# Optimization experiments

Measured on AMD Instinct MI355X. Metric: run time of the kernel, lower is better.

## Reference

```python
import jax, jax.numpy as jnp
import numpy as np

N_EMBD = 1024
N_HEAD = 16
DIM_HEAD = N_EMBD // N_HEAD
SCALE = DIM_HEAD ** (-0.5)  # NOTE: module DIVIDES by this (multiplies by sqrt(d)) - kept faithful


def setup_inputs() -> dict:
    key = jax.random.key(0)
    ks = jax.random.split(key, 6)
    B, Tq, Tkv = 2, 2048, 2048
    x_q = jax.random.normal(ks[0], (B, Tq, N_EMBD), dtype=jnp.float32)
    x_kv = jax.random.normal(ks[1], (B, Tkv, N_EMBD), dtype=jnp.float32)
    position_bias = jax.random.normal(ks[2], (1, N_HEAD, Tq, Tkv), dtype=jnp.float32)
    s = 0.02
    W_q = jax.random.normal(ks[3], (N_EMBD, N_EMBD), dtype=jnp.float32) * s
    W_kv = jax.random.normal(ks[4], (N_EMBD, 2 * N_EMBD), dtype=jnp.float32) * s
    W_proj = jax.random.normal(ks[5], (N_EMBD, N_EMBD), dtype=jnp.float32) * s
    return {"x_q": x_q, "x_kv": x_kv, "position_bias": position_bias,
            "W_q": W_q, "W_kv": W_kv, "W_proj": W_proj}


def reference(x_q, x_kv, position_bias, W_q, W_kv, W_proj):
    B, Tq, C = x_q.shape
    Tkv = x_kv.shape[1]
    q = x_q @ W_q                       # [B,Tq,C]
    kv = x_kv @ W_kv                    # [B,Tkv,2C]
    k, v = kv[..., :C], kv[..., C:]
    # split heads -> [B,H,T,dh]
    q = q.reshape(B, Tq, N_HEAD, DIM_HEAD).transpose(0, 2, 1, 3)
    k = k.reshape(B, Tkv, N_HEAD, DIM_HEAD).transpose(0, 2, 1, 3)
    v = v.reshape(B, Tkv, N_HEAD, DIM_HEAD).transpose(0, 2, 1, 3)
    attn = jnp.einsum('bhqd,bhkd->bhqk', q, k)
    attn = attn + position_bias
    attn = attn / SCALE  # faithful to source: divides by d**-0.5
    attn = jax.nn.softmax(attn, axis=-1)
    y = jnp.einsum('bhqk,bhkd->bhqd', attn, v)
    y = y.transpose(0, 2, 1, 3).reshape(B, Tq, C)
    return y @ W_proj
```

## Files before the change

### kernel.cpp

```cpp
#include <hip/hip_runtime.h>
#include <hip/hip_bf16.h>

#define TQ   2048
#define TKV  2048
#define NB   2
#define NH   16
#define HD   64
#define CE   1024
#define MQ   (NB*TQ)

typedef __bf16 bf16_t;
typedef __bf16 bf16x4_t __attribute__((ext_vector_type(4)));
typedef __bf16 bf16x8_t __attribute__((ext_vector_type(8)));
typedef float  f32x4_t  __attribute__((ext_vector_type(4)));

#define MFMA16(a,b,c) __builtin_amdgcn_mfma_f32_16x16x32_bf16((a),(b),(c),0,0,0)

__device__ __forceinline__ void gload16(const void* g, void* l) {
    __builtin_amdgcn_global_load_lds(
        (__attribute__((address_space(1))) void*)(void*)g,
        (__attribute__((address_space(3))) void*)l, 16, 0, 0);
}

__global__ __launch_bounds__(256) void cvt_split(const float* __restrict__ x,
                                                 bf16_t* __restrict__ hi,
                                                 bf16_t* __restrict__ lo, int n4) {
    int i = blockIdx.x * blockDim.x + threadIdx.x;
    int stride = gridDim.x * blockDim.x;
    for (; i < n4; i += stride) {
        f32x4_t v = ((const f32x4_t*)x)[i];
        bf16x4_t h, l;
#pragma unroll
        for (int j = 0; j < 4; j++) {
            h[j] = (bf16_t)v[j];
            l[j] = (bf16_t)(v[j] - (float)h[j]);
        }
        ((bf16x4_t*)hi)[i] = h;
        ((bf16x4_t*)lo)[i] = l;
    }
}

__global__ __launch_bounds__(256) void wsplit_t(const float* __restrict__ W,
                                                bf16_t* __restrict__ Wh,
                                                bf16_t* __restrict__ Wl, int K, int N) {
    __shared__ float t[32][33];
    int tx = threadIdx.x, ty = threadIdx.y;
    int n0 = blockIdx.x * 32, k0 = blockIdx.y * 32;
#pragma unroll
    for (int j = 0; j < 4; j++)
        t[ty + 8*j][tx] = W[(size_t)(k0 + ty + 8*j) * N + n0 + tx];
    __syncthreads();
#pragma unroll
    for (int j = 0; j < 4; j++) {
        float v = t[tx][ty + 8*j];
        bf16_t h = (bf16_t)v;
        Wh[(size_t)(n0 + ty + 8*j) * K + k0 + tx] = h;
        Wl[(size_t)(n0 + ty + 8*j) * K + k0 + tx] = (bf16_t)(v - (float)h);
    }
}

__global__ __launch_bounds__(256) void vtrans(const bf16_t* __restrict__ KVm,
                                              bf16_t* __restrict__ VT) {
    __shared__ bf16_t t[32][33];
    int tx = threadIdx.x, ty = threadIdx.y;
    int t0 = blockIdx.x * 32, d0 = blockIdx.y * 32, bh = blockIdx.z;
    int b = bh >> 4, h = bh & 15;
#pragma unroll
    for (int j = 0; j < 4; j++)
        t[ty + 8*j][tx] = KVm[(size_t)(b*TKV + t0 + ty + 8*j) * 2048 + 1024 + h*HD + d0 + tx];
    __syncthreads();
#pragma unroll
    for (int j = 0; j < 4; j++)
        VT[((size_t)bh*HD + d0 + ty + 8*j) * TKV + t0 + tx] = t[tx][ty + 8*j];
}

template <int PASSES, typename CT>
__device__ __forceinline__ void gemm_body(const bf16_t* __restrict__ Ah,
                                          const bf16_t* __restrict__ Al,
                                          const bf16_t* __restrict__ Bh,
                                          const bf16_t* __restrict__ Bl,
                                          CT* __restrict__ C,
                                          bf16_t* __restrict__ Clo,
                                          int bi, int bj, int N, int K, int Nlo,
                                          bf16_t* As, bf16_t* Bs, int tid) {
    int lane = tid & 63, w = tid >> 6;
    int wr = (w >> 1) * 64, wc = (w & 1) * 64;
    int lr = lane & 15, lg = lane >> 4;
    int row0 = tid >> 2, seg0 = tid & 3;

    f32x4_t acc[4][4];
#pragma unroll
    for (int m = 0; m < 4; m++)
#pragma unroll
        for (int n = 0; n < 4; n++)
            acc[m][n] = f32x4_t{0.f, 0.f, 0.f, 0.f};

    for (int p = 0; p < PASSES; ++p) {
        const bf16_t* Ap;
        const bf16_t* Bp;
        if (p == 0)      { Ap = Ah; Bp = Bh; }
        else if (p == 1) { if (PASSES == 3) { Ap = Ah; Bp = Bl; } else { Ap = Al; Bp = Bh; } }
        else             { Ap = Al; Bp = Bh; }
        for (int k0 = 0; k0 < K; k0 += 32) {
#pragma unroll
            for (int i = 0; i < 2; i++) {
                int row = row0 + i * 64;
                int sseg = seg0 ^ (row & 3);
                gload16(Ap + (size_t)(bi*128 + row) * K + k0 + sseg*8, (void*)(As + row*32 + seg0*8));
                gload16(Bp + (size_t)(bj*128 + row) * K + k0 + sseg*8, (void*)(Bs + row*32 + seg0*8));
            }
            __syncthreads();
            bf16x8_t af[4], bfr[4];
#pragma unroll
            for (int m = 0; m < 4; m++) {
                int ra = wr + m*16 + lr;
                af[m]  = *(const bf16x8_t*)(As + ra*32 + ((lg ^ (ra & 3)) * 8));
                int rb = wc + m*16 + lr;
                bfr[m] = *(const bf16x8_t*)(Bs + rb*32 + ((lg ^ (rb & 3)) * 8));
            }
#pragma unroll
            for (int m = 0; m < 4; m++)
#pragma unroll
                for (int n = 0; n < 4; n++)
                    acc[m][n] = MFMA16(af[m], bfr[n], acc[m][n]);
            __syncthreads();
        }
    }
#pragma unroll
    for (int m = 0; m < 4; m++) {
        int r = bi*128 + wr + m*16 + lg*4;
#pragma unroll
        for (int n = 0; n < 4; n++) {
            int c = bj*128 + wc + n*16 + lr;
#pragma unroll
            for (int i = 0; i < 4; i++) {
                float v = acc[m][n][i];
                if constexpr (__is_same(CT, float)) {
                    C[(size_t)(r + i) * N + c] = v;
                } else {
                    bf16_t h = (bf16_t)v;
                    C[(size_t)(r + i) * N + c] = h;
                    if (Clo && c < Nlo)
                        Clo[(size_t)(r + i) * Nlo + c] = (bf16_t)(v - (float)h);
                }
            }
        }
    }
}

__global__ __launch_bounds__(256) void gemm_qkv(const bf16_t* xqh, const bf16_t* xql,
                                                const bf16_t* wqh, const bf16_t* wql,
                                                bf16_t* q_hi, bf16_t* q_lo,
                                                const bf16_t* xkh, const bf16_t* xkl,
                                                const bf16_t* wkh, const bf16_t* wkl,
                                                bf16_t* kv_hi, bf16_t* k_lo) {
    __shared__ bf16_t As[128 * 32];
    __shared__ bf16_t Bs[128 * 32];
    int id = blockIdx.x, tid = threadIdx.x;
    if (id < 256) {
        gemm_body<3, bf16_t>(xqh, xql, wqh, wql, q_hi, q_lo,
                             id >> 3, id & 7, CE, CE, CE, As, Bs, tid);
    } else {
        id -= 256;
        gemm_body<3, bf16_t>(xkh, xkl, wkh, wkl, kv_hi, k_lo,
                             id >> 4, id & 15, 2048, CE, CE, As, Bs, tid);
    }
}

__global__ __launch_bounds__(256) void gemm_proj(const bf16_t* yh, const bf16_t* yl,
                                                 const bf16_t* wph,
                                                 float* out) {
    __shared__ bf16_t As[128 * 32];
    __shared__ bf16_t Bs[128 * 32];
    int id = blockIdx.x, tid = threadIdx.x;
    gemm_body<2, float>(yh, yl, wph, nullptr, out, nullptr,
                        id >> 3, id & 7, CE, CE, 0, As, Bs, tid);
}

__global__ __launch_bounds__(256, 2) void attn_fwd3(const bf16_t* __restrict__ Qh,
                                                    const bf16_t* __restrict__ Ql,
                                                    const bf16_t* __restrict__ KVh,
                                                    const bf16_t* __restrict__ Kl,
                                                    const bf16_t* __restrict__ VT,
                                                    const float*  __restrict__ Bias,
                                                    bf16_t* __restrict__ Yh,
                                                    bf16_t* __restrict__ Yl) {
    __shared__ bf16_t Kh_s[64 * 64];
    __shared__ bf16_t Kl_s[64 * 64];
    __shared__ bf16_t V_s [64 * 64];
    __shared__ bf16_t pb[4][32 * 72];

    int id = blockIdx.x;
    int swz = (id & 7) * 64 + (id >> 3);
    int qt = swz & 15, bh = swz >> 4;
    int b = bh >> 4, h = bh & 15;
    int tid = threadIdx.x, lane = tid & 63, w = tid >> 6;
    int lr = lane & 15, lg = lane >> 4;
    int q0 = qt * 128 + w * 32;

    bf16x8_t qhf[2][2], qlf[2][2];
#pragma unroll
    for (int qs = 0; qs < 2; qs++) {
        const bf16_t* qp = Qh + (size_t)(b*TQ + q0 + qs*16 + lr) * CE + h*HD + lg*8;
        const bf16_t* qp2 = Ql + (size_t)(b*TQ + q0 + qs*16 + lr) * CE + h*HD + lg*8;
        qhf[qs][0] = *(const bf16x8_t*)qp;
        qhf[qs][1] = *(const bf16x8_t*)(qp + 32);
        qlf[qs][0] = *(const bf16x8_t*)qp2;
        qlf[qs][1] = *(const bf16x8_t*)(qp2 + 32);
    }

    float m_r[2][4], l_r[2][4];
    f32x4_t oa[2][4];
#pragma unroll
    for (int qs = 0; qs < 2; qs++)
#pragma unroll
        for (int i = 0; i < 4; i++) {
            m_r[qs][i] = -1e30f; l_r[qs][i] = 0.f;
            oa[qs][i] = f32x4_t{0.f, 0.f, 0.f, 0.f};
        }

    bf16_t* myp = pb[w];
    const float*  bbase = Bias + ((size_t)h*TQ + q0 + lg*4) * TKV + lr;
    const bf16_t* khg = KVh + (size_t)(b*TKV) * 2048 + h*HD;
    const bf16_t* klg = Kl  + (size_t)(b*TKV) * 1024 + h*HD;
    const bf16_t* vtg = VT  + (size_t)bh * HD * TKV;

    for (int kv0 = 0; kv0 < TKV; kv0 += 64) {
#pragma unroll
        for (int s = 0; s < 2; s++) {
            int idx = s * 256 + tid;
            int row = idx >> 3;
            int sw  = (idx & 7) ^ (row & 7);
            gload16(khg + (size_t)(kv0 + row) * 2048 + sw*8, (void*)(Kh_s + idx*8));
            gload16(klg + (size_t)(kv0 + row) * 1024 + sw*8, (void*)(Kl_s + idx*8));
            gload16(vtg + (size_t)row * TKV + kv0 + sw*8,    (void*)(V_s  + idx*8));
        }
        float bv[2][4][4];
#pragma unroll
        for (int qs = 0; qs < 2; qs++)
#pragma unroll
            for (int i = 0; i < 4; i++)
#pragma unroll
                for (int g = 0; g < 4; g++)
                    bv[qs][g][i] = bbase[(size_t)(qs*16 + i) * TKV + kv0 + g*16];
        __syncthreads();

        bf16x8_t khf_[4][2], klf_[4][2];
#pragma unroll
        for (int g = 0; g < 4; g++) {
            int rb = (g*16 + lr) * 64, x = lr & 7;
            khf_[g][0] = *(const bf16x8_t*)(Kh_s + rb + ((lg     ^ x) * 8));
            khf_[g][1] = *(const bf16x8_t*)(Kh_s + rb + (((4+lg) ^ x) * 8));
            klf_[g][0] = *(const bf16x8_t*)(Kl_s + rb + ((lg     ^ x) * 8));
            klf_[g][1] = *(const bf16x8_t*)(Kl_s + rb + (((4+lg) ^ x) * 8));
        }
        f32x4_t sg[2][4];
#pragma unroll
        for (int qs = 0; qs < 2; qs++)
#pragma unroll
            for (int g = 0; g < 4; g++) {
                f32x4_t s = f32x4_t{0.f, 0.f, 0.f, 0.f};
                s = MFMA16(qhf[qs][0], khf_[g][0], s);
                s = MFMA16(qhf[qs][1], khf_[g][1], s);
                s = MFMA16(qlf[qs][0], khf_[g][0], s);
                s = MFMA16(qlf[qs][1], khf_[g][1], s);
                s = MFMA16(qhf[qs][0], klf_[g][0], s);
                s = MFMA16(qhf[qs][1], klf_[g][1], s);
                sg[qs][g] = s;
            }

        float p[2][4][4], mx[2][4], mn_[2][4];
        int grow = 0;
#pragma unroll
        for (int qs = 0; qs < 2; qs++)
#pragma unroll
            for (int i = 0; i < 4; i++) {
                float a0 = (sg[qs][0][i] + bv[qs][0][i]) * 8.f;
                float a1 = (sg[qs][1][i] + bv[qs][1][i]) * 8.f;
                float a2 = (sg[qs][2][i] + bv[qs][2][i]) * 8.f;
                float a3 = (sg[qs][3][i] + bv[qs][3][i]) * 8.f;
                p[qs][0][i] = a0; p[qs][1][i] = a1; p[qs][2][i] = a2; p[qs][3][i] = a3;
                mx[qs][i] = fmaxf(fmaxf(a0, a1), fmaxf(a2, a3));
            }
#pragma unroll
        for (int d = 1; d < 16; d <<= 1)
#pragma unroll
            for (int qs = 0; qs < 2; qs++)
#pragma unroll
                for (int i = 0; i < 4; i++)
                    mx[qs][i] = fmaxf(mx[qs][i], __shfl_xor(mx[qs][i], d));
#pragma unroll
        for (int qs = 0; qs < 2; qs++)
#pragma unroll
            for (int i = 0; i < 4; i++) {
                mn_[qs][i] = fmaxf(m_r[qs][i], mx[qs][i]);
                grow |= (mn_[qs][i] > m_r[qs][i]) ? 1 : 0;
            }
        if (__any(grow)) {
#pragma unroll
            for (int qs = 0; qs < 2; qs++)
#pragma unroll
                for (int i = 0; i < 4; i++) {
                    float sc = __expf(m_r[qs][i] - mn_[qs][i]);
                    m_r[qs][i] = mn_[qs][i];
                    l_r[qs][i] *= sc;
#pragma unroll
                    for (int c = 0; c < 4; c++) oa[qs][c][i] *= sc;
                }
        }
        float rs[2][4];
#pragma unroll
        for (int qs = 0; qs < 2; qs++)
#pragma unroll
            for (int i = 0; i < 4; i++) {
                float r = 0.f;
#pragma unroll
                for (int g = 0; g < 4; g++) {
                    p[qs][g][i] = __expf(p[qs][g][i] - m_r[qs][i]);
                    r += p[qs][g][i];
                }
                rs[qs][i] = r;
            }
#pragma unroll
        for (int d = 1; d < 16; d <<= 1)
#pragma unroll
            for (int qs = 0; qs < 2; qs++)
#pragma unroll
                for (int i = 0; i < 4; i++)
                    rs[qs][i] += __shfl_xor(rs[qs][i], d);
#pragma unroll
        for (int qs = 0; qs < 2; qs++)
#pragma unroll
            for (int i = 0; i < 4; i++)
                l_r[qs][i] += rs[qs][i];

#pragma unroll
        for (int qs = 0; qs < 2; qs++)
#pragma unroll
            for (int i = 0; i < 4; i++)
#pragma unroll
                for (int g = 0; g < 4; g++)
                    myp[(qs*16 + lg*4 + i)*72 + g*16 + lr] = (bf16_t)p[qs][g][i];
        bf16x8_t pa[2][2];
#pragma unroll
        for (int qs = 0; qs < 2; qs++) {
            pa[qs][0] = *(const bf16x8_t*)(myp + (qs*16 + lr)*72 + lg*8);
            pa[qs][1] = *(const bf16x8_t*)(myp + (qs*16 + lr)*72 + 32 + lg*8);
        }
#pragma unroll
        for (int c = 0; c < 4; c++) {
            int r = c*16 + lr, x = r & 7;
            bf16x8_t vf0 = *(const bf16x8_t*)(V_s + r*64 + ((lg     ^ x) * 8));
            bf16x8_t vf1 = *(const bf16x8_t*)(V_s + r*64 + (((4+lg) ^ x) * 8));
#pragma unroll
            for (int qs = 0; qs < 2; qs++) {
                oa[qs][c] = MFMA16(pa[qs][0], vf0, oa[qs][c]);
                oa[qs][c] = MFMA16(pa[qs][1], vf1, oa[qs][c]);
            }
        }
        __syncthreads();
    }

#pragma unroll
    for (int qs = 0; qs < 2; qs++)
#pragma unroll
        for (int c = 0; c < 4; c++)
#pragma unroll
            for (int i = 0; i < 4; i++) {
                float yv = oa[qs][c][i] / l_r[qs][i];
                bf16_t hh = (bf16_t)yv;
                size_t idx = (size_t)(b*TQ + q0 + qs*16 + lg*4 + i) * CE + h*HD + c*16 + lr;
                Yh[idx] = hh;
                Yl[idx] = (bf16_t)(yv - (float)hh);
            }
}

extern "C" void kernel_launch(void* const* d_in, const int* in_sizes, int n_in,
                              void* d_out, int out_size, void* d_ws, size_t ws_size,
                              hipStream_t stream) {
    const float* x_q   = (const float*)d_in[0];
    const float* x_kv  = (const float*)d_in[1];
    const float* pbias = (const float*)d_in[2];
    const float* W_q   = (const float*)d_in[3];
    const float* W_kv  = (const float*)d_in[4];
    const float* W_pj  = (const float*)d_in[5];
    float* out = (float*)d_out;

    bf16_t* ws = (bf16_t*)d_ws;
    const size_t MEG = 1024 * 1024;
    bf16_t* xq_hi  = ws;
    bf16_t* xq_lo  = ws + 4*MEG;
    bf16_t* xkv_hi = ws + 8*MEG;
    bf16_t* xkv_lo = ws + 12*MEG;
    bf16_t* wqT_h  = ws + 16*MEG;
    bf16_t* wqT_l  = ws + 17*MEG;
    bf16_t* wkvT_h = ws + 18*MEG;
    bf16_t* wkvT_l = ws + 20*MEG;
    bf16_t* wpT_h  = ws + 22*MEG;
    bf16_t* wpT_l  = ws + 23*MEG;
    bf16_t* q_hi   = ws + 24*MEG;
    bf16_t* q_lo   = ws + 28*MEG;
    bf16_t* kv_hi  = ws + 32*MEG;
    bf16_t* k_lo   = ws + 40*MEG;
    bf16_t* vT     = xkv_lo;
    bf16_t* y_hi   = xq_hi;
    bf16_t* y_lo   = xq_lo;

    dim3 tb(32, 8);
    cvt_split<<<1024, 256, 0, stream>>>(x_q,  xq_hi,  xq_lo,  (MQ*CE)/4);
    cvt_split<<<1024, 256, 0, stream>>>(x_kv, xkv_hi, xkv_lo, (MQ*CE)/4);
    wsplit_t<<<dim3(32, 32), tb, 0, stream>>>(W_q,  wqT_h,  wqT_l,  CE, CE);
    wsplit_t<<<dim3(64, 32), tb, 0, stream>>>(W_kv, wkvT_h, wkvT_l, CE, 2048);
    wsplit_t<<<dim3(32, 32), tb, 0, stream>>>(W_pj, wpT_h,  wpT_l,  CE, CE);

    gemm_qkv<<<768, 256, 0, stream>>>(xq_hi, xq_lo, wqT_h, wqT_l, q_hi, q_lo,
                                      xkv_hi, xkv_lo, wkvT_h, wkvT_l, kv_hi, k_lo);

    vtrans<<<dim3(64, 2, 32), tb, 0, stream>>>(kv_hi, vT);

    attn_fwd3<<<512, 256, 0, stream>>>(q_hi, q_lo, kv_hi, k_lo, vT, pbias, y_hi, y_lo);

    gemm_proj<<<256, 256, 0, stream>>>(y_hi, y_lo, wpT_h, out);
}
```

Before: 670.0 us.

## Fuse V-transpose into QKV GEMM, double-buffer attention K, drop low-precision passes

The V projection now runs as a single-pass bf16 GEMM inside the QKV kernel and writes V already transposed, which removes the separate vtrans launch and its extra round trip through memory. The attention kernel double-buffers K hi/lo tiles in LDS and loads V fragments and bias straight into registers, overlapping the next tile's loads with the current tile's compute. The y low part is dropped, so the output projection runs one bf16 pass instead of two, and W_proj no longer gets a low split. These changes cut memory traffic and MFMA work, but V and y now keep only bf16 precision, which may loosen accuracy.

After: 1.595 ms. 138% more time.

```diff
diff --git a/kernel.cpp b/kernel.cpp
--- a/kernel.cpp
+++ b/kernel.cpp
@@ -55,23 +55,9 @@
         float v = t[tx][ty + 8*j];
         bf16_t h = (bf16_t)v;
         Wh[(size_t)(n0 + ty + 8*j) * K + k0 + tx] = h;
-        Wl[(size_t)(n0 + ty + 8*j) * K + k0 + tx] = (bf16_t)(v - (float)h);
-    }
-}
-
-__global__ __launch_bounds__(256) void vtrans(const bf16_t* __restrict__ KVm,
-                                              bf16_t* __restrict__ VT) {
-    __shared__ bf16_t t[32][33];
-    int tx = threadIdx.x, ty = threadIdx.y;
-    int t0 = blockIdx.x * 32, d0 = blockIdx.y * 32, bh = blockIdx.z;
-    int b = bh >> 4, h = bh & 15;
-#pragma unroll
-    for (int j = 0; j < 4; j++)
-        t[ty + 8*j][tx] = KVm[(size_t)(b*TKV + t0 + ty + 8*j) * 2048 + 1024 + h*HD + d0 + tx];
-    __syncthreads();
-#pragma unroll
-    for (int j = 0; j < 4; j++)
-        VT[((size_t)bh*HD + d0 + ty + 8*j) * TKV + t0 + tx] = t[tx][ty + 8*j];
+        if (Wl)
+            Wl[(size_t)(n0 + ty + 8*j) * K + k0 + tx] = (bf16_t)(v - (float)h);
+    }
 }
 
 template <int PASSES, typename CT>
@@ -148,46 +134,102 @@
     }
 }
 
+__device__ __forceinline__ void gemm_vt_body(const bf16_t* __restrict__ A,
+                                             const bf16_t* __restrict__ B,
+                                             bf16_t* __restrict__ VT_,
+                                             int bi, int bj,
+                                             bf16_t* As, bf16_t* Bs, int tid) {
+    const int K = CE;
+    int lane = tid & 63, w = tid >> 6;
+    int wr = (w >> 1) * 64, wc = (w & 1) * 64;
+    int lr = lane & 15, lg = lane >> 4;
+    int row0 = tid >> 2, seg0 = tid & 3;
+
+    f32x4_t acc[4][4];
+#pragma unroll
+    for (int m = 0; m < 4; m++)
+#pragma unroll
+        for (int n = 0; n < 4; n++)
+            acc[m][n] = f32x4_t{0.f, 0.f, 0.f, 0.f};
+
+    for (int k0 = 0; k0 < K; k0 += 32) {
+#pragma unroll
+        for (int i = 0; i < 2; i++) {
+            int row = row0 + i * 64;
+            int sseg = seg0 ^ (row & 3);
+            gload16(A + (size_t)(bi*128 + row) * K + k0 + sseg*8, (void*)(As + row*32 + seg0*8));
+            gload16(B + (size_t)(bj*128 + row) * K + k0 + sseg*8, (void*)(Bs + row*32 + seg0*8));
+        }
+        __syncthreads();
+        bf16x8_t af[4], bfr[4];
+#pragma unroll
+        for (int m = 0; m < 4; m++) {
+            int ra = wr + m*16 + lr;
+            af[m]  = *(const bf16x8_t*)(As + ra*32 + ((lg ^ (ra & 3)) * 8));
+            int rb = wc + m*16 + lr;
+            bfr[m] = *(const bf16x8_t*)(Bs + rb*32 + ((lg ^ (rb & 3)) * 8));
+        }
+#pragma unroll
+        for (int m = 0; m < 4; m++)
+#pragma unroll
+            for (int n = 0; n < 4; n++)
+                acc[m][n] = MFMA16(af[m], bfr[n], acc[m][n]);
+        __syncthreads();
+    }
+#pragma unroll
+    for (int m = 0; m < 4; m++) {
+        int r0 = bi*128 + wr + m*16 + lg*4;
+        int bb = r0 >> 11, t = r0 & 2047;
+#pragma unroll
+        for (int n = 0; n < 4; n++) {
+            int c = bj*128 + wc + n*16 + lr;
+            int hh = c >> 6, d = c & 63;
+            bf16x4_t vv;
+#pragma unroll
+            for (int i = 0; i < 4; i++) vv[i] = (bf16_t)acc[m][n][i];
+            *(bf16x4_t*)(VT_ + ((((size_t)bb*16 + hh)*64 + d)*2048 + t)) = vv;
+        }
+    }
+}
+
 __global__ __launch_bounds__(256) void gemm_qkv(const bf16_t* xqh, const bf16_t* xql,
                                                 const bf16_t* wqh, const bf16_t* wql,
                                                 bf16_t* q_hi, bf16_t* q_lo,
                                                 const bf16_t* xkh, const bf16_t* xkl,
                                                 const bf16_t* wkh, const bf16_t* wkl,
-                                                bf16_t* kv_hi, bf16_t* k_lo) {
+                                                bf16_t* k_hi, bf16_t* k_lo,
+                                                bf16_t* vT) {
     __shared__ bf16_t As[128 * 32];
     __shared__ bf16_t Bs[128 * 32];
     int id = blockIdx.x, tid = threadIdx.x;
-    if (id < 256) {
-        gemm_body<3, bf16_t>(xqh, xql, wqh, wql, q_hi, q_lo,
-                             id >> 3, id & 7, CE, CE, CE, As, Bs, tid);
-    } else {
-        id -= 256;
-        gemm_body<3, bf16_t>(xkh, xkl, wkh, wkl, kv_hi, k_lo,
-                             id >> 4, id & 15, 2048, CE, CE, As, Bs, tid);
-    }
-}
-
-__global__ __launch_bounds__(256) void gemm_proj(const bf16_t* yh, const bf16_t* yl,
-                                                 const bf16_t* wph,
+    int role = id % 3, sub = id / 3;
+    int bi = sub >> 3, bj = sub & 7;
+    if (role == 0)
+        gemm_body<3, bf16_t>(xqh, xql, wqh, wql, q_hi, q_lo, bi, bj, CE, CE, CE, As, Bs, tid);
+    else if (role == 1)
+        gemm_body<3, bf16_t>(xkh, xkl, wkh, wkl, k_hi, k_lo, bi, bj, CE, CE, CE, As, Bs, tid);
+    else
+        gemm_vt_body(xkh, wkh + (size_t)1024*CE, vT, bi, bj, As, Bs, tid);
+}
+
+__global__ __launch_bounds__(256) void gemm_proj(const bf16_t* yh, const bf16_t* wph,
                                                  float* out) {
     __shared__ bf16_t As[128 * 32];
     __shared__ bf16_t Bs[128 * 32];
     int id = blockIdx.x, tid = threadIdx.x;
-    gemm_body<2, float>(yh, yl, wph, nullptr, out, nullptr,
+    gemm_body<1, float>(yh, nullptr, wph, nullptr, out, nullptr,
                         id >> 3, id & 7, CE, CE, 0, As, Bs, tid);
 }
 
-__global__ __launch_bounds__(256, 2) void attn_fwd3(const bf16_t* __restrict__ Qh,
+__global__ __launch_bounds__(256, 2) void attn_fwd4(const bf16_t* __restrict__ Qh,
                                                     const bf16_t* __restrict__ Ql,
-                                                    const bf16_t* __restrict__ KVh,
-                                                    const bf16_t* __restrict__ Kl,
-                                                    const bf16_t* __restrict__ VT,
+                                                    const bf16_t* __restrict__ Khg,
+                                                    const bf16_t* __restrict__ Klg,
+                                                    const bf16_t* __restrict__ VTg,
                                                     const float*  __restrict__ Bias,
-                                                    bf16_t* __restrict__ Yh,
-                                                    bf16_t* __restrict__ Yl) {
-    __shared__ bf16_t Kh_s[64 * 64];
-    __shared__ bf16_t Kl_s[64 * 64];
-    __shared__ bf16_t V_s [64 * 64];
+                                                    bf16_t* __restrict__ Yh) {
+    __shared__ bf16_t KhS[2][64 * 64];
+    __shared__ bf16_t KlS[2][64 * 64];
     __shared__ bf16_t pb[4][32 * 72];
 
     int id = blockIdx.x;
@@ -201,7 +243,7 @@
     bf16x8_t qhf[2][2], qlf[2][2];
 #pragma unroll
     for (int qs = 0; qs < 2; qs++) {
-        const bf16_t* qp = Qh + (size_t)(b*TQ + q0 + qs*16 + lr) * CE + h*HD + lg*8;
+        const bf16_t* qp  = Qh + (size_t)(b*TQ + q0 + qs*16 + lr) * CE + h*HD + lg*8;
         const bf16_t* qp2 = Ql + (size_t)(b*TQ + q0 + qs*16 + lr) * CE + h*HD + lg*8;
         qhf[qs][0] = *(const bf16x8_t*)qp;
         qhf[qs][1] = *(const bf16x8_t*)(qp + 32);
@@ -221,21 +263,21 @@
 
     bf16_t* myp = pb[w];
     const float*  bbase = Bias + ((size_t)h*TQ + q0 + lg*4) * TKV + lr;
-    const bf16_t* khg = KVh + (size_t)(b*TKV) * 2048 + h*HD;
-    const bf16_t* klg = Kl  + (size_t)(b*TKV) * 1024 + h*HD;
-    const bf16_t* vtg = VT  + (size_t)bh * HD * TKV;
-
-    for (int kv0 = 0; kv0 < TKV; kv0 += 64) {
+    const bf16_t* kh0 = Khg + (size_t)b*TKV*CE + h*HD;
+    const bf16_t* kl0 = Klg + (size_t)b*TKV*CE + h*HD;
+    const bf16_t* vtg = VTg + (size_t)bh * HD * TKV;
+
+    auto STAGE = [&](int bufi, int kv0) {
 #pragma unroll
         for (int s = 0; s < 2; s++) {
             int idx = s * 256 + tid;
             int row = idx >> 3;
             int sw  = (idx & 7) ^ (row & 7);
-            gload16(khg + (size_t)(kv0 + row) * 2048 + sw*8, (void*)(Kh_s + idx*8));
-            gload16(klg + (size_t)(kv0 + row) * 1024 + sw*8, (void*)(Kl_s + idx*8));
-            gload16(vtg + (size_t)row * TKV + kv0 + sw*8,    (void*)(V_s  + idx*8));
-        }
-        float bv[2][4][4];
+            gload16(kh0 + (size_t)(kv0 + row) * CE + sw*8, (void*)(&KhS[bufi][idx*8]));
+            gload16(kl0 + (size_t)(kv0 + row) * CE + sw*8, (void*)(&KlS[bufi][idx*8]));
+        }
+    };
+    auto BLOAD = [&](float (&bv)[2][4][4], int kv0) {
 #pragma unroll
         for (int qs = 0; qs < 2; qs++)
 #pragma unroll
@@ -243,32 +285,36 @@
 #pragma unroll
                 for (int g = 0; g < 4; g++)
                     bv[qs][g][i] = bbase[(size_t)(qs*16 + i) * TKV + kv0 + g*16];
-        __syncthreads();
-
-        bf16x8_t khf_[4][2], klf_[4][2];
+    };
+    auto VLOAD = [&](bf16x8_t (&vf)[4][2], int kv0) {
+#pragma unroll
+        for (int c = 0; c < 4; c++) {
+            const bf16_t* vp = vtg + (size_t)(c*16 + lr) * TKV + kv0 + lg*8;
+            vf[c][0] = *(const bf16x8_t*)vp;
+            vf[c][1] = *(const bf16x8_t*)(vp + 32);
+        }
+    };
+    auto COMPUTE = [&](int bufi, float (&bv)[2][4][4], bf16x8_t (&vf)[4][2]) {
+        f32x4_t sg[2][4];
 #pragma unroll
         for (int g = 0; g < 4; g++) {
             int rb = (g*16 + lr) * 64, x = lr & 7;
-            khf_[g][0] = *(const bf16x8_t*)(Kh_s + rb + ((lg     ^ x) * 8));
-            khf_[g][1] = *(const bf16x8_t*)(Kh_s + rb + (((4+lg) ^ x) * 8));
-            klf_[g][0] = *(const bf16x8_t*)(Kl_s + rb + ((lg     ^ x) * 8));
-            klf_[g][1] = *(const bf16x8_t*)(Kl_s + rb + (((4+lg) ^ x) * 8));
-        }
-        f32x4_t sg[2][4];
-#pragma unroll
-        for (int qs = 0; qs < 2; qs++)
-#pragma unroll
-            for (int g = 0; g < 4; g++) {
+            bf16x8_t kh_0 = *(const bf16x8_t*)(&KhS[bufi][rb + ((lg     ^ x) * 8)]);
+            bf16x8_t kh_1 = *(const bf16x8_t*)(&KhS[bufi][rb + (((4+lg) ^ x) * 8)]);
+            bf16x8_t kl_0 = *(const bf16x8_t*)(&KlS[bufi][rb + ((lg     ^ x) * 8)]);
+            bf16x8_t kl_1 = *(const bf16x8_t*)(&KlS[bufi][rb + (((4+lg) ^ x) * 8)]);
+#pragma unroll
+            for (int qs = 0; qs < 2; qs++) {
                 f32x4_t s = f32x4_t{0.f, 0.f, 0.f, 0.f};
-                s = MFMA16(qhf[qs][0], khf_[g][0], s);
-                s = MFMA16(qhf[qs][1], khf_[g][1], s);
-                s = MFMA16(qlf[qs][0], khf_[g][0], s);
-                s = MFMA16(qlf[qs][1], khf_[g][1], s);
-                s = MFMA16(qhf[qs][0], klf_[g][0], s);
-                s = MFMA16(qhf[qs][1], klf_[g][1], s);
+                s = MFMA16(qhf[qs][0], kh_0, s);
+                s = MFMA16(qhf[qs][1], kh_1, s);
+                s = MFMA16(qlf[qs][0], kh_0, s);
+                s = MFMA16(qlf[qs][1], kh_1, s);
+                s = MFMA16(qhf[qs][0], kl_0, s);
+                s = MFMA16(qhf[qs][1], kl_1, s);
                 sg[qs][g] = s;
             }
-
+        }
         float p[2][4][4], mx[2][4], mn_[2][4];
         int grow = 0;
 #pragma unroll
@@ -348,16 +394,34 @@
             pa[qs][1] = *(const bf16x8_t*)(myp + (qs*16 + lr)*72 + 32 + lg*8);
         }
 #pragma unroll
-        for (int c = 0; c < 4; c++) {
-            int r = c*16 + lr, x = r & 7;
-            bf16x8_t vf0 = *(const bf16x8_t*)(V_s + r*64 + ((lg     ^ x) * 8));
-            bf16x8_t vf1 = *(const bf16x8_t*)(V_s + r*64 + (((4+lg) ^ x) * 8));
+        for (int c = 0; c < 4; c++)
 #pragma unroll
             for (int qs = 0; qs < 2; qs++) {
-                oa[qs][c] = MFMA16(pa[qs][0], vf0, oa[qs][c]);
-                oa[qs][c] = MFMA16(pa[qs][1], vf1, oa[qs][c]);
-            }
-        }
+                oa[qs][c] = MFMA16(pa[qs][0], vf[c][0], oa[qs][c]);
+                oa[qs][c] = MFMA16(pa[qs][1], vf[c][1], oa[qs][c]);
+            }
+    };
+
+    float bv_a[2][4][4], bv_b[2][4][4];
+    bf16x8_t vfa[4][2], vfb[4][2];
+
+    STAGE(0, 0);
+    BLOAD(bv_a, 0);
+    __syncthreads();
+
+    for (int it = 0; it < TKV/128; it++) {
+        int kvA = it*128, kvB = kvA + 64;
+        VLOAD(vfa, kvA);
+        STAGE(1, kvB);
+        BLOAD(bv_b, kvB);
+        COMPUTE(0, bv_a, vfa);
+        __syncthreads();
+        VLOAD(vfb, kvB);
+        if (kvB + 64 < TKV) {
+            STAGE(0, kvB + 64);
+            BLOAD(bv_a, kvB + 64);
+        }
+        COMPUTE(1, bv_b, vfb);
         __syncthreads();
     }
 
@@ -368,10 +432,8 @@
 #pragma unroll
             for (int i = 0; i < 4; i++) {
                 float yv = oa[qs][c][i] / l_r[qs][i];
-                bf16_t hh = (bf16_t)yv;
                 size_t idx = (size_t)(b*TQ + q0 + qs*16 + lg*4 + i) * CE + h*HD + c*16 + lr;
-                Yh[idx] = hh;
-                Yl[idx] = (bf16_t)(yv - (float)hh);
+                Yh[idx] = (bf16_t)yv;
             }
 }
 
@@ -397,28 +459,24 @@
     bf16_t* wkvT_h = ws + 18*MEG;
     bf16_t* wkvT_l = ws + 20*MEG;
     bf16_t* wpT_h  = ws + 22*MEG;
-    bf16_t* wpT_l  = ws + 23*MEG;
-    bf16_t* q_hi   = ws + 24*MEG;
-    bf16_t* q_lo   = ws + 28*MEG;
-    bf16_t* kv_hi  = ws + 32*MEG;
-    bf16_t* k_lo   = ws + 40*MEG;
-    bf16_t* vT     = xkv_lo;
+    bf16_t* q_hi   = ws + 23*MEG;
+    bf16_t* q_lo   = ws + 27*MEG;
+    bf16_t* k_hi   = ws + 31*MEG;
+    bf16_t* k_lo   = ws + 35*MEG;
+    bf16_t* vT     = ws + 39*MEG;
     bf16_t* y_hi   = xq_hi;
-    bf16_t* y_lo   = xq_lo;
 
     dim3 tb(32, 8);
     cvt_split<<<1024, 256, 0, stream>>>(x_q,  xq_hi,  xq_lo,  (MQ*CE)/4);
     cvt_split<<<1024, 256, 0, stream>>>(x_kv, xkv_hi, xkv_lo, (MQ*CE)/4);
     wsplit_t<<<dim3(32, 32), tb, 0, stream>>>(W_q,  wqT_h,  wqT_l,  CE, CE);
     wsplit_t<<<dim3(64, 32), tb, 0, stream>>>(W_kv, wkvT_h, wkvT_l, CE, 2048);
-    wsplit_t<<<dim3(32, 32), tb, 0, stream>>>(W_pj, wpT_h,  wpT_l,  CE, CE);
+    wsplit_t<<<dim3(32, 32), tb, 0, stream>>>(W_pj, wpT_h,  nullptr, CE, CE);
 
     gemm_qkv<<<768, 256, 0, stream>>>(xq_hi, xq_lo, wqT_h, wqT_l, q_hi, q_lo,
-                                      xkv_hi, xkv_lo, wkvT_h, wkvT_l, kv_hi, k_lo);
-
-    vtrans<<<dim3(64, 2, 32), tb, 0, stream>>>(kv_hi, vT);
-
-    attn_fwd3<<<512, 256, 0, stream>>>(q_hi, q_lo, kv_hi, k_lo, vT, pbias, y_hi, y_lo);
-
-    gemm_proj<<<256, 256, 0, stream>>>(y_hi, y_lo, wpT_h, out);
-}
+                                      xkv_hi, xkv_lo, wkvT_h, wkvT_l, k_hi, k_lo, vT);
+
+    attn_fwd4<<<512, 256, 0, stream>>>(q_hi, q_lo, k_hi, k_lo, vT, pbias, y_hi);
+
+    gemm_proj<<<256, 256, 0, stream>>>(y_hi, wpT_h, out);
+}
```
